# Optimization experiments

Hardware: AMD Instinct MI355X
Metric: run time of the kernel (lower is better)

Reference implementation:

```python
import jax, jax.numpy as jnp
import numpy as np

N_NODES = 2048
N_EDGES = 8192
EDGE_DIM = 10
EDGE_HIDDEN = 32
HID = 160


def nnconv(x, edge_index, edge_attr, w1, b1, w2, b2, root, bias):
    """PyG-style NNConv with aggr='mean'.
    x: [N, HID], edge_attr: [E, EDGE_DIM], edge_index: [2, E] (src, dst).
    Per-edge weight W_e = MLP(e) reshaped to [HID, HID]; message = x[src] @ W_e,
    mean-aggregated at dst, plus root transform and bias.
    """
    n = x.shape[0]
    h = jax.nn.relu(edge_attr @ w1 + b1)                     # [E, EDGE_HIDDEN]
    W = (h @ w2 + b2).reshape(-1, HID, HID)                  # [E, HID, HID]
    src, dst = edge_index[0], edge_index[1]
    msg = jnp.einsum('ei,eio->eo', x[src], W)                # [E, HID]
    summed = jax.ops.segment_sum(msg, dst, num_segments=n)   # [N, HID]
    cnt = jax.ops.segment_sum(jnp.ones((msg.shape[0],), x.dtype), dst,
                              num_segments=n)
    aggr = summed / jnp.maximum(cnt, 1.0)[:, None]           # mean; 0 for isolated
    return aggr + x @ root + bias


def setup_inputs() -> dict:
    key = jax.random.key(0)
    ks = jax.random.split(key, 16)
    s = 1.0 / np.sqrt(HID)
    se = 1.0 / np.sqrt(EDGE_DIM)
    sh = 1.0 / np.sqrt(EDGE_HIDDEN)
    inp = {
        'x': jax.random.normal(ks[0], (N_NODES, HID), jnp.float32),
        'edge_attr': jax.random.uniform(ks[1], (N_EDGES, EDGE_DIM), jnp.float32),
        # conv1 (subgraph_conv1) params
        'w1_a': jax.random.normal(ks[2], (EDGE_DIM, EDGE_HIDDEN), jnp.float32) * se,
        'b1_a': jnp.zeros((EDGE_HIDDEN,), jnp.float32),
        'w2_a': jax.random.normal(ks[3], (EDGE_HIDDEN, HID * HID), jnp.float32) * sh,
        'b2_a': jnp.zeros((HID * HID,), jnp.float32),
        'root_a': jax.random.normal(ks[4], (HID, HID), jnp.float32) * s,
        'bias_a': jnp.zeros((HID,), jnp.float32),
        # conv2 (subgraph_conv2, applied twice) params
        'w1_b': jax.random.normal(ks[5], (EDGE_DIM, EDGE_HIDDEN), jnp.float32) * se,
        'b1_b': jnp.zeros((EDGE_HIDDEN,), jnp.float32),
        'w2_b': jax.random.normal(ks[6], (EDGE_HIDDEN, HID * HID), jnp.float32) * sh,
        'b2_b': jnp.zeros((HID * HID,), jnp.float32),
        'root_b': jax.random.normal(ks[7], (HID, HID), jnp.float32) * s,
        'bias_b': jnp.zeros((HID,), jnp.float32),
        'edge_index': jax.random.randint(ks[8], (2, N_EDGES), 0, N_NODES, jnp.int64),
    }
    return inp


def reference(x, edge_attr, w1_a, b1_a, w2_a, b2_a, root_a, bias_a,
              w1_b, b1_b, w2_b, b2_b, root_b, bias_b, edge_index):
    # subgraph_conv1 -> ReLU -> subgraph_conv2 -> ReLU -> subgraph_conv2
    h = jax.nn.relu(nnconv(x, edge_index, edge_attr,
                           w1_a, b1_a, w2_a, b2_a, root_a, bias_a))
    h = jax.nn.relu(nnconv(h, edge_index, edge_attr,
                           w1_b, b1_b, w2_b, b2_b, root_b, bias_b))
    h = nnconv(h, edge_index, edge_attr,
               w1_b, b1_b, w2_b, b2_b, root_b, bias_b)
    return h
```

## Files before the change

### kernel.cpp

```cpp
#include <hip/hip_runtime.h>

#define NN 2048
#define NE 8192
#define ED 10
#define EH 32
#define HID 160
#define KT 5440
#define KS 10
#define KSTEPS 17

typedef __attribute__((ext_vector_type(8))) short short8;
typedef __attribute__((ext_vector_type(4))) float f32x4;
typedef unsigned int u32;

__device__ __forceinline__ ushort f2bf(float v) {
    u32 u = __float_as_uint(v);
    u += 0x7FFF + ((u >> 16) & 1);
    return (ushort)(u >> 16);
}
__device__ __forceinline__ float bf2f(ushort u) {
    return __uint_as_float(((u32)u) << 16);
}
__device__ __forceinline__ void gl2lds16(const ushort* g, ushort* l) {
    __builtin_amdgcn_global_load_lds(
        (const __attribute__((address_space(1))) u32*)g,
        (__attribute__((address_space(3))) u32*)l, 16, 0, 0);
}

__global__ __launch_bounds__(256) void k_prep(
        const float* __restrict__ x, ushort* __restrict__ xb,
        const float* __restrict__ ea,
        const float* __restrict__ w1a, const float* __restrict__ b1a,
        const float* __restrict__ w1b, const float* __restrict__ b1b,
        float* __restrict__ ha, float* __restrict__ hb,
        const float* __restrict__ w2a, const float* __restrict__ b2a,
        const float* __restrict__ roota,
        const float* __restrict__ w2b, const float* __restrict__ b2b,
        const float* __restrict__ rootb,
        ushort* __restrict__ WcA, ushort* __restrict__ WcB,
        const int* __restrict__ ei, int* __restrict__ doff,
        int* __restrict__ degg, float* __restrict__ dinv,
        int* __restrict__ delist) {
    __shared__ __align__(16) char smem[21760];
    int b = blockIdx.x, t = threadIdx.x;

    if (b < 512) {
        int set = b >> 8, rel = b & 255;
        const float* w1 = set ? w1b : w1a;
        const float* b1 = set ? b1b : b1a;
        float* h = set ? hb : ha;
        int idx = rel * 1024 + t * 4;
        int e = idx >> 5, j0 = idx & 31;
        float o4[4];
#pragma unroll
        for (int u = 0; u < 4; ++u) {
            float acc = b1[j0 + u];
#pragma unroll
            for (int i = 0; i < ED; ++i) acc += ea[e * ED + i] * w1[i * EH + j0 + u];
            o4[u] = fmaxf(acc, 0.f);
        }
        *(float4*)&h[idx] = *(const float4*)o4;
        return;
    }
    if (b < 672) {
        int rel = b - 512;
        int set = rel / 80, i0 = (rel % 80) * 2;
        u32 (*tile)[34] = (u32(*)[34])smem;
        const float* w2 = set ? w2b : w2a;
        const float* b2 = set ? b2b : b2a;
        const float* root = set ? rootb : roota;
        ushort* W = set ? WcB : WcA;
        if (t < HID) {
#pragma unroll
            for (int di = 0; di < 2; ++di) {
                int i = i0 + di;
#pragma unroll
                for (int p = 0; p < 16; ++p) {
                    float v0 = w2[(size_t)(2 * p) * 25600 + i * HID + t];
                    float v1 = w2[(size_t)(2 * p + 1) * 25600 + i * HID + t];
                    tile[t][di * 17 + p] = ((u32)f2bf(v1) << 16) | f2bf(v0);
                }
                tile[t][di * 17 + 16] = ((u32)f2bf(root[i * HID + t]) << 16) |
                                        f2bf(b2[i * HID + t]);
            }
        }
        __syncthreads();
        u32* dst = (u32*)W;
        for (int w = t; w < 5440; w += 256) {
            int o = w / 34, j = w - o * 34;
            dst[(size_t)o * 2720 + i0 * 17 + j] = tile[o][j];
        }
        return;
    }
    if (b < 992) {
        int idx = (b - 672) * 1024 + t * 4;
        float4 xv = *(const float4*)&x[idx];
        ushort o4[4] = {f2bf(xv.x), f2bf(xv.y), f2bf(xv.z), f2bf(xv.w)};
        *(u32*)&xb[idx] = *(const u32*)&o4[0];
        *(u32*)&xb[idx + 2] = *(const u32*)&o4[2];
        return;
    }
    int* deg = (int*)smem;
    int* cur = deg + NN;
    int* part = cur + NN;
    for (int i = t; i < NN; i += 256) deg[i] = 0;
    __syncthreads();
    for (int e = t; e < NE; e += 256) atomicAdd(&deg[ei[NE + e]], 1);
    __syncthreads();
    int loc[8], s = 0;
#pragma unroll
    for (int i = 0; i < 8; ++i) { loc[i] = s; s += deg[t * 8 + i]; }
    part[t] = s;
    __syncthreads();
    int tot = s;
    for (int st = 1; st < 256; st <<= 1) {
        int v = (t >= st) ? part[t - st] : 0;
        __syncthreads();
        part[t] += v;
        __syncthreads();
    }
    int base = part[t] - tot;
#pragma unroll
    for (int i = 0; i < 8; ++i) {
        int d = t * 8 + i;
        doff[d] = base + loc[i];
        cur[d] = base + loc[i];
        degg[d] = deg[d];
        dinv[d] = 1.0f / fmaxf((float)deg[d], 1.0f);
    }
    __syncthreads();
    for (int e = t; e < NE; e += 256) {
        int d = ei[NE + e];
        int p = atomicAdd(&cur[d], 1);
        delist[p] = e;
    }
}

__global__ __launch_bounds__(160) void k_scatter(
        const ushort* __restrict__ xb, const float* __restrict__ h,
        const int* __restrict__ ei, const int* __restrict__ doff,
        const int* __restrict__ degg, const float* __restrict__ dinv,
        const int* __restrict__ delist, ushort* __restrict__ T) {
    __shared__ float hbuf[32 * EH];
    __shared__ int ebuf[32], sbuf[32];
    __shared__ u32 rowbuf[KT / 2];
    int d = blockIdx.x, t = threadIdx.x;
    int o0 = doff[d], dg = degg[d];
    float acc[33];
#pragma unroll
    for (int q = 0; q < 33; ++q) acc[q] = 0.f;
    for (int c0 = 0; c0 < dg; c0 += 32) {
        int nc = min(32, dg - c0);
        __syncthreads();
        if (t < nc) {
            int e = delist[o0 + c0 + t];
            ebuf[t] = e;
            sbuf[t] = ei[e];
        }
        __syncthreads();
        for (int i = t; i < nc * EH; i += 160)
            hbuf[i] = h[(size_t)ebuf[i >> 5] * EH + (i & 31)];
        __syncthreads();
        for (int j = 0; j < nc; ++j) {
            float xs = bf2f(xb[(size_t)sbuf[j] * HID + t]);
            const float* hj = &hbuf[j * EH];
#pragma unroll
            for (int q = 0; q < 32; ++q) acc[q] += hj[q] * xs;
            acc[32] += xs;
        }
    }
    float di = dinv[d];
#pragma unroll
    for (int p = 0; p < 16; ++p)
        rowbuf[t * 17 + p] = ((u32)f2bf(acc[2 * p + 1] * di) << 16) |
                             f2bf(acc[2 * p] * di);
    rowbuf[t * 17 + 16] = ((u32)xb[(size_t)d * HID + t] << 16) | f2bf(acc[32] * di);
    __syncthreads();
    u32* Trow = (u32*)(T + (size_t)d * KT);
    for (int w = t; w < KT / 2; w += 160) Trow[w] = rowbuf[w];
}

__global__ __launch_bounds__(256) void k_out(const ushort* __restrict__ A,
                                             const ushort* __restrict__ B,
                                             float* __restrict__ Cp) {
    __shared__ ushort sA[2][128 * 32], sB[2][160 * 32];
    int tid = threadIdx.x;
    int bm = blockIdx.x * 128, ks = blockIdx.y;
    int k0base = ks * (KT / KS);
    int wid = tid >> 6, lane = tid & 63;
    int wm = (wid >> 1) * 64, wn = (wid & 1) * 80;
    int lr = lane & 15, lk = lane >> 4;
    f32x4 acc[4][5];
#pragma unroll
    for (int i = 0; i < 4; ++i)
#pragma unroll
        for (int j = 0; j < 5; ++j) acc[i][j] = (f32x4){0.f, 0.f, 0.f, 0.f};

    auto stage = [&](int buf, int c) {
        int k0 = k0base + c * 32;
#pragma unroll
        for (int i = 0; i < 2; ++i) {
            int s = tid + i * 256;
            int r = s >> 2, go = (s & 3) * 8;
            gl2lds16(&A[(size_t)(bm + r) * KT + k0 + go], &sA[buf][s * 8]);
        }
#pragma unroll
        for (int i = 0; i < 2; ++i) {
            int s = tid + i * 256;
            int r = s >> 2, go = (s & 3) * 8;
            gl2lds16(&B[(size_t)r * KT + k0 + go], &sB[buf][s * 8]);
        }
        if (tid < 128) {
            int s = tid + 512;
            int r = s >> 2, go = (s & 3) * 8;
            gl2lds16(&B[(size_t)r * KT + k0 + go], &sB[buf][s * 8]);
        }
    };
    stage(0, 0);
    __syncthreads();
    for (int c = 0; c < KSTEPS; ++c) {
        int cur = c & 1;
        if (c + 1 < KSTEPS) stage(cur ^ 1, c + 1);
        short8 av[4], bv[5];
#pragma unroll
        for (int mt = 0; mt < 4; ++mt)
            av[mt] = *(const short8*)&sA[cur][(wm + mt * 16 + lr) * 32 + lk * 8];
#pragma unroll
        for (int nt = 0; nt < 5; ++nt)
            bv[nt] = *(const short8*)&sB[cur][(wn + nt * 16 + lr) * 32 + lk * 8];
#pragma unroll
        for (int mt = 0; mt < 4; ++mt)
#pragma unroll
            for (int nt = 0; nt < 5; ++nt)
                acc[mt][nt] = __builtin_amdgcn_mfma_f32_16x16x32_bf16(
                    av[mt], bv[nt], acc[mt][nt], 0, 0, 0);
        __syncthreads();
    }
    float* Cb = Cp + (size_t)ks * NN * HID;
#pragma unroll
    for (int mt = 0; mt < 4; ++mt)
#pragma unroll
        for (int nt = 0; nt < 5; ++nt) {
            int m0 = bm + wm + mt * 16 + lk * 4;
            int n = wn + nt * 16 + lr;
#pragma unroll
            for (int r = 0; r < 4; ++r)
                Cb[(size_t)(m0 + r) * HID + n] = acc[mt][nt][r];
        }
}

__global__ __launch_bounds__(160) void k_fin(const float* __restrict__ Cp,
        const float* __restrict__ bias, ushort* __restrict__ xn,
        float* __restrict__ out, int last) {
    int d = blockIdx.x, t = threadIdx.x;
    float s = bias[t];
#pragma unroll
    for (int p = 0; p < KS; ++p) s += Cp[(size_t)p * NN * HID + d * HID + t];
    if (last) out[d * HID + t] = s;
    else      xn[d * HID + t] = f2bf(fmaxf(s, 0.f));
}

extern "C" void kernel_launch(void* const* d_in, const int* in_sizes, int n_in,
                              void* d_out, int out_size, void* d_ws, size_t ws_size,
                              hipStream_t stream) {
    const float* x     = (const float*)d_in[0];
    const float* ea    = (const float*)d_in[1];
    const float* w1a   = (const float*)d_in[2];
    const float* b1a   = (const float*)d_in[3];
    const float* w2a   = (const float*)d_in[4];
    const float* b2a   = (const float*)d_in[5];
    const float* roota = (const float*)d_in[6];
    const float* biasa = (const float*)d_in[7];
    const float* w1b   = (const float*)d_in[8];
    const float* b1b   = (const float*)d_in[9];
    const float* w2b   = (const float*)d_in[10];
    const float* b2b   = (const float*)d_in[11];
    const float* rootb = (const float*)d_in[12];
    const float* biasb = (const float*)d_in[13];
    const int*   ei    = (const int*)d_in[14];
    float* out = (float*)d_out;

    char* p = (char*)d_ws;
    ushort* T   = (ushort*)p;  p += (size_t)NN * KT * 2;
    ushort* WcA = (ushort*)p;  p += (size_t)HID * KT * 2;
    ushort* WcB = (ushort*)p;  p += (size_t)HID * KT * 2;
    float* Cp   = (float*)p;   p += (size_t)KS * NN * HID * 4;
    float* h_a  = (float*)p;   p += (size_t)NE * EH * 4;
    float* h_b  = (float*)p;   p += (size_t)NE * EH * 4;
    ushort* xb0 = (ushort*)p;  p += (size_t)NN * HID * 2;
    ushort* xn  = (ushort*)p;  p += (size_t)NN * HID * 2;
    int* doff   = (int*)p;     p += NN * 4;
    int* degg   = (int*)p;     p += NN * 4;
    float* dinv = (float*)p;   p += NN * 4;
    int* delist = (int*)p;     p += NE * 4;

    k_prep<<<993, 256, 0, stream>>>(x, xb0, ea, w1a, b1a, w1b, b1b, h_a, h_b,
                                    w2a, b2a, roota, w2b, b2b, rootb, WcA, WcB,
                                    ei, doff, degg, dinv, delist);

    struct Layer { const ushort *xin, *wc; const float *h, *bias; int last; };
    Layer L[3] = {
        {xb0, WcA, h_a, biasa, 0},
        {xn,  WcB, h_b, biasb, 0},
        {xn,  WcB, h_b, biasb, 1},
    };
    for (int l = 0; l < 3; ++l) {
        k_scatter<<<NN, 160, 0, stream>>>(L[l].xin, L[l].h, ei, doff, degg,
                                          dinv, delist, T);
        k_out<<<dim3(NN / 128, KS), 256, 0, stream>>>(T, L[l].wc, Cp);
        k_fin<<<NN, 160, 0, stream>>>(Cp, L[l].bias, xn, out, L[l].last);
    }
}
```

Before: 201.1 us.

## Fuse scatter, GEMM and finalize into one per-layer kernel split by K-slices

Replaces the per-layer scatter + GEMM + finalize chain with a single kernel per layer. Each block handles 32 destination nodes and one 16-wide input-channel slice. It builds its slice of the aggregated A operand directly in LDS and runs the MFMA GEMM against the streamed weight slice, writing K-split partials. The next layer reconstructs its input by summing the previous partials plus bias and ReLU during the gather, which removes the large T intermediate and the bf16 x buffers. The cost is that the gather now reads ten fp32 partials per source element, and each block only does a 32-row GEMM that re-streams the weights.

```diff
diff --git a/kernel.cpp b/kernel.cpp
--- a/kernel.cpp
+++ b/kernel.cpp
@@ -7,7 +7,10 @@
 #define HID 160
 #define KT 5440
 #define KS 10
-#define KSTEPS 17
+#define KSL 544
+#define MT 32
+#define APAD 552
+#define NNH (NN * HID)
 
 typedef __attribute__((ext_vector_type(8))) short short8;
 typedef __attribute__((ext_vector_type(4))) float f32x4;
@@ -21,14 +24,26 @@
 __device__ __forceinline__ float bf2f(ushort u) {
     return __uint_as_float(((u32)u) << 16);
 }
+__device__ __forceinline__ u32 packbf(float lo, float hi) {
+    return ((u32)f2bf(hi) << 16) | f2bf(lo);
+}
 __device__ __forceinline__ void gl2lds16(const ushort* g, ushort* l) {
     __builtin_amdgcn_global_load_lds(
         (const __attribute__((address_space(1))) u32*)g,
         (__attribute__((address_space(3))) u32*)l, 16, 0, 0);
 }
 
+__device__ __forceinline__ float gatherx(const float* __restrict__ x0,
+                                         const float* __restrict__ cpin,
+                                         float biasv, int node, int i) {
+    if (x0) return x0[node * HID + i];
+    float s = biasv;
+#pragma unroll
+    for (int p = 0; p < KS; ++p) s += cpin[(size_t)p * NNH + node * HID + i];
+    return fmaxf(s, 0.f);
+}
+
 __global__ __launch_bounds__(256) void k_prep(
-        const float* __restrict__ x, ushort* __restrict__ xb,
         const float* __restrict__ ea,
         const float* __restrict__ w1a, const float* __restrict__ b1a,
         const float* __restrict__ w1b, const float* __restrict__ b1b,
@@ -78,10 +93,9 @@
                 for (int p = 0; p < 16; ++p) {
                     float v0 = w2[(size_t)(2 * p) * 25600 + i * HID + t];
                     float v1 = w2[(size_t)(2 * p + 1) * 25600 + i * HID + t];
-                    tile[t][di * 17 + p] = ((u32)f2bf(v1) << 16) | f2bf(v0);
+                    tile[t][di * 17 + p] = packbf(v0, v1);
                 }
-                tile[t][di * 17 + 16] = ((u32)f2bf(root[i * HID + t]) << 16) |
-                                        f2bf(b2[i * HID + t]);
+                tile[t][di * 17 + 16] = packbf(b2[i * HID + t], root[i * HID + t]);
             }
         }
         __syncthreads();
@@ -90,14 +104,6 @@
             int o = w / 34, j = w - o * 34;
             dst[(size_t)o * 2720 + i0 * 17 + j] = tile[o][j];
         }
-        return;
-    }
-    if (b < 992) {
-        int idx = (b - 672) * 1024 + t * 4;
-        float4 xv = *(const float4*)&x[idx];
-        ushort o4[4] = {f2bf(xv.x), f2bf(xv.y), f2bf(xv.z), f2bf(xv.w)};
-        *(u32*)&xb[idx] = *(const u32*)&o4[0];
-        *(u32*)&xb[idx + 2] = *(const u32*)&o4[2];
         return;
     }
     int* deg = (int*)smem;
@@ -136,128 +142,139 @@
     }
 }
 
-__global__ __launch_bounds__(160) void k_scatter(
-        const ushort* __restrict__ xb, const float* __restrict__ h,
+__global__ __launch_bounds__(256) void k_layer(
+        const float* __restrict__ x0,
+        const float* __restrict__ cpin,
+        const float* __restrict__ bprev,
+        const float* __restrict__ h, const ushort* __restrict__ wc,
         const int* __restrict__ ei, const int* __restrict__ doff,
         const int* __restrict__ degg, const float* __restrict__ dinv,
-        const int* __restrict__ delist, ushort* __restrict__ T) {
-    __shared__ float hbuf[32 * EH];
-    __shared__ int ebuf[32], sbuf[32];
-    __shared__ u32 rowbuf[KT / 2];
-    int d = blockIdx.x, t = threadIdx.x;
-    int o0 = doff[d], dg = degg[d];
-    float acc[33];
-#pragma unroll
-    for (int q = 0; q < 33; ++q) acc[q] = 0.f;
-    for (int c0 = 0; c0 < dg; c0 += 32) {
-        int nc = min(32, dg - c0);
+        const int* __restrict__ delist, float* __restrict__ cpout) {
+    __shared__ __align__(16) ushort sA[MT * APAD];
+    __shared__ __align__(16) ushort sB[2][160 * 32];
+    __shared__ float hbuf[128 * 33];
+    __shared__ int ebuf[128], sbuf[128];
+    int t = threadIdx.x;
+    int bm = blockIdx.x, ks = blockIdx.y;
+    int d0 = bm * MT, i0 = ks * 16;
+    int e0 = doff[d0];
+    int e1 = (d0 + MT < NN) ? doff[d0 + MT] : NE;
+
+    int il = t & 15, i = i0 + il;
+    int dA = d0 + (t >> 4), dB = dA + 16;
+    float biasv = x0 ? 0.f : bprev[i];
+    int aLo = doff[dA], aHi = aLo + degg[dA];
+    int bLo = doff[dB], bHi = bLo + degg[dB];
+    float accA[33], accB[33];
+#pragma unroll
+    for (int q = 0; q < 33; ++q) { accA[q] = 0.f; accB[q] = 0.f; }
+
+    for (int c0 = e0; c0 < e1; c0 += 128) {
+        int nc = min(128, e1 - c0);
         __syncthreads();
         if (t < nc) {
-            int e = delist[o0 + c0 + t];
+            int e = delist[c0 + t];
             ebuf[t] = e;
             sbuf[t] = ei[e];
         }
         __syncthreads();
-        for (int i = t; i < nc * EH; i += 160)
-            hbuf[i] = h[(size_t)ebuf[i >> 5] * EH + (i & 31)];
-        __syncthreads();
-        for (int j = 0; j < nc; ++j) {
-            float xs = bf2f(xb[(size_t)sbuf[j] * HID + t]);
-            const float* hj = &hbuf[j * EH];
-#pragma unroll
-            for (int q = 0; q < 32; ++q) acc[q] += hj[q] * xs;
-            acc[32] += xs;
-        }
-    }
-    float di = dinv[d];
-#pragma unroll
-    for (int p = 0; p < 16; ++p)
-        rowbuf[t * 17 + p] = ((u32)f2bf(acc[2 * p + 1] * di) << 16) |
-                             f2bf(acc[2 * p] * di);
-    rowbuf[t * 17 + 16] = ((u32)xb[(size_t)d * HID + t] << 16) | f2bf(acc[32] * di);
-    __syncthreads();
-    u32* Trow = (u32*)(T + (size_t)d * KT);
-    for (int w = t; w < KT / 2; w += 160) Trow[w] = rowbuf[w];
-}
-
-__global__ __launch_bounds__(256) void k_out(const ushort* __restrict__ A,
-                                             const ushort* __restrict__ B,
-                                             float* __restrict__ Cp) {
-    __shared__ ushort sA[2][128 * 32], sB[2][160 * 32];
-    int tid = threadIdx.x;
-    int bm = blockIdx.x * 128, ks = blockIdx.y;
-    int k0base = ks * (KT / KS);
-    int wid = tid >> 6, lane = tid & 63;
-    int wm = (wid >> 1) * 64, wn = (wid & 1) * 80;
-    int lr = lane & 15, lk = lane >> 4;
-    f32x4 acc[4][5];
-#pragma unroll
-    for (int i = 0; i < 4; ++i)
-#pragma unroll
-        for (int j = 0; j < 5; ++j) acc[i][j] = (f32x4){0.f, 0.f, 0.f, 0.f};
+        for (int idx = t; idx < nc * 32; idx += 256)
+            hbuf[(idx >> 5) * 33 + (idx & 31)] =
+                h[(size_t)ebuf[idx >> 5] * EH + (idx & 31)];
+        __syncthreads();
+        int jl = max(aLo, c0) - c0, jh = min(aHi, c0 + nc) - c0;
+        for (int j = jl; j < jh; ++j) {
+            float xs = gatherx(x0, cpin, biasv, sbuf[j], i);
+            const float* hj = &hbuf[j * 33];
+#pragma unroll
+            for (int q = 0; q < 32; ++q) accA[q] += hj[q] * xs;
+            accA[32] += xs;
+        }
+        jl = max(bLo, c0) - c0; jh = min(bHi, c0 + nc) - c0;
+        for (int j = jl; j < jh; ++j) {
+            float xs = gatherx(x0, cpin, biasv, sbuf[j], i);
+            const float* hj = &hbuf[j * 33];
+#pragma unroll
+            for (int q = 0; q < 32; ++q) accB[q] += hj[q] * xs;
+            accB[32] += xs;
+        }
+    }
+    float rootA = gatherx(x0, cpin, biasv, dA, i);
+    float rootB = gatherx(x0, cpin, biasv, dB, i);
 
     auto stage = [&](int buf, int c) {
-        int k0 = k0base + c * 32;
-#pragma unroll
-        for (int i = 0; i < 2; ++i) {
-            int s = tid + i * 256;
+        size_t k0 = (size_t)ks * KSL + c * 32;
+#pragma unroll
+        for (int q = 0; q < 2; ++q) {
+            int s = t + q * 256;
             int r = s >> 2, go = (s & 3) * 8;
-            gl2lds16(&A[(size_t)(bm + r) * KT + k0 + go], &sA[buf][s * 8]);
-        }
-#pragma unroll
-        for (int i = 0; i < 2; ++i) {
-            int s = tid + i * 256;
+            gl2lds16(&wc[(size_t)r * KT + k0 + go], &sB[buf][s * 8]);
+        }
+        if (t < 128) {
+            int s = t + 512;
             int r = s >> 2, go = (s & 3) * 8;
-            gl2lds16(&B[(size_t)r * KT + k0 + go], &sB[buf][s * 8]);
-        }
-        if (tid < 128) {
-            int s = tid + 512;
-            int r = s >> 2, go = (s & 3) * 8;
-            gl2lds16(&B[(size_t)r * KT + k0 + go], &sB[buf][s * 8]);
+            gl2lds16(&wc[(size_t)r * KT + k0 + go], &sB[buf][s * 8]);
         }
     };
     stage(0, 0);
-    __syncthreads();
-    for (int c = 0; c < KSTEPS; ++c) {
+
+    {
+        float diA = dinv[dA], diB = dinv[dB];
+        u32* pa = (u32*)&sA[(t >> 4) * APAD + il * 34];
+        u32* pb = (u32*)&sA[((t >> 4) + 16) * APAD + il * 34];
+#pragma unroll
+        for (int p = 0; p < 16; ++p) {
+            pa[p] = packbf(accA[2 * p] * diA, accA[2 * p + 1] * diA);
+            pb[p] = packbf(accB[2 * p] * diB, accB[2 * p + 1] * diB);
+        }
+        pa[16] = packbf(accA[32] * diA, rootA);
+        pb[16] = packbf(accB[32] * diB, rootB);
+    }
+    __syncthreads();
+
+    int wid = t >> 6, lane = t & 63;
+    int wm = (wid >> 1) * 16, wn = (wid & 1) * 80;
+    int lr = lane & 15, lk = lane >> 4;
+    f32x4 acc[5];
+#pragma unroll
+    for (int j = 0; j < 5; ++j) acc[j] = (f32x4){0.f, 0.f, 0.f, 0.f};
+
+    for (int c = 0; c < 17; ++c) {
         int cur = c & 1;
-        if (c + 1 < KSTEPS) stage(cur ^ 1, c + 1);
-        short8 av[4], bv[5];
-#pragma unroll
-        for (int mt = 0; mt < 4; ++mt)
-            av[mt] = *(const short8*)&sA[cur][(wm + mt * 16 + lr) * 32 + lk * 8];
+        if (c + 1 < 17) stage(cur ^ 1, c + 1);
+        short8 av = *(const short8*)&sA[(wm + lr) * APAD + c * 32 + lk * 8];
+        short8 bv[5];
 #pragma unroll
         for (int nt = 0; nt < 5; ++nt)
             bv[nt] = *(const short8*)&sB[cur][(wn + nt * 16 + lr) * 32 + lk * 8];
 #pragma unroll
-        for (int mt = 0; mt < 4; ++mt)
-#pragma unroll
-            for (int nt = 0; nt < 5; ++nt)
-                acc[mt][nt] = __builtin_amdgcn_mfma_f32_16x16x32_bf16(
-                    av[mt], bv[nt], acc[mt][nt], 0, 0, 0);
-        __syncthreads();
-    }
-    float* Cb = Cp + (size_t)ks * NN * HID;
-#pragma unroll
-    for (int mt = 0; mt < 4; ++mt)
-#pragma unroll
-        for (int nt = 0; nt < 5; ++nt) {
-            int m0 = bm + wm + mt * 16 + lk * 4;
-            int n = wn + nt * 16 + lr;
-#pragma unroll
-            for (int r = 0; r < 4; ++r)
-                Cb[(size_t)(m0 + r) * HID + n] = acc[mt][nt][r];
-        }
-}
-
-__global__ __launch_bounds__(160) void k_fin(const float* __restrict__ Cp,
-        const float* __restrict__ bias, ushort* __restrict__ xn,
-        float* __restrict__ out, int last) {
-    int d = blockIdx.x, t = threadIdx.x;
-    float s = bias[t];
-#pragma unroll
-    for (int p = 0; p < KS; ++p) s += Cp[(size_t)p * NN * HID + d * HID + t];
-    if (last) out[d * HID + t] = s;
-    else      xn[d * HID + t] = f2bf(fmaxf(s, 0.f));
+        for (int nt = 0; nt < 5; ++nt)
+            acc[nt] = __builtin_amdgcn_mfma_f32_16x16x32_bf16(av, bv[nt], acc[nt], 0, 0, 0);
+        __syncthreads();
+    }
+
+    float* Cb = cpout + (size_t)ks * NNH;
+#pragma unroll
+    for (int nt = 0; nt < 5; ++nt) {
+        int n = wn + nt * 16 + lr;
+        int m0 = d0 + wm + lk * 4;
+#pragma unroll
+        for (int r = 0; r < 4; ++r)
+            Cb[(size_t)(m0 + r) * HID + n] = acc[nt][r];
+    }
+}
+
+__global__ __launch_bounds__(256) void k_fin(const float* __restrict__ Cp,
+                                             const float* __restrict__ bias,
+                                             float* __restrict__ out) {
+    int base = (blockIdx.x * 256 + threadIdx.x) * 4;
+    float4 s = *(const float4*)&bias[base % HID];
+#pragma unroll
+    for (int p = 0; p < KS; ++p) {
+        float4 v = *(const float4*)&Cp[(size_t)p * NNH + base];
+        s.x += v.x; s.y += v.y; s.z += v.z; s.w += v.w;
+    }
+    *(float4*)&out[base] = s;
 }
 
 extern "C" void kernel_launch(void* const* d_in, const int* in_sizes, int n_in,
@@ -281,33 +298,27 @@
     float* out = (float*)d_out;
 
     char* p = (char*)d_ws;
-    ushort* T   = (ushort*)p;  p += (size_t)NN * KT * 2;
+    float* Cp0  = (float*)p;   p += (size_t)KS * NNH * 4;
+    float* Cp1  = (float*)p;   p += (size_t)KS * NNH * 4;
     ushort* WcA = (ushort*)p;  p += (size_t)HID * KT * 2;
     ushort* WcB = (ushort*)p;  p += (size_t)HID * KT * 2;
-    float* Cp   = (float*)p;   p += (size_t)KS * NN * HID * 4;
     float* h_a  = (float*)p;   p += (size_t)NE * EH * 4;
     float* h_b  = (float*)p;   p += (size_t)NE * EH * 4;
-    ushort* xb0 = (ushort*)p;  p += (size_t)NN * HID * 2;
-    ushort* xn  = (ushort*)p;  p += (size_t)NN * HID * 2;
     int* doff   = (int*)p;     p += NN * 4;
     int* degg   = (int*)p;     p += NN * 4;
     float* dinv = (float*)p;   p += NN * 4;
     int* delist = (int*)p;     p += NE * 4;
 
-    k_prep<<<993, 256, 0, stream>>>(x, xb0, ea, w1a, b1a, w1b, b1b, h_a, h_b,
+    k_prep<<<673, 256, 0, stream>>>(ea, w1a, b1a, w1b, b1b, h_a, h_b,
                                     w2a, b2a, roota, w2b, b2b, rootb, WcA, WcB,
                                     ei, doff, degg, dinv, delist);
 
-    struct Layer { const ushort *xin, *wc; const float *h, *bias; int last; };
-    Layer L[3] = {
-        {xb0, WcA, h_a, biasa, 0},
-        {xn,  WcB, h_b, biasb, 0},
-        {xn,  WcB, h_b, biasb, 1},
-    };
-    for (int l = 0; l < 3; ++l) {
-        k_scatter<<<NN, 160, 0, stream>>>(L[l].xin, L[l].h, ei, doff, degg,
-                                          dinv, delist, T);
-        k_out<<<dim3(NN / 128, KS), 256, 0, stream>>>(T, L[l].wc, Cp);
-        k_fin<<<NN, 160, 0, stream>>>(Cp, L[l].bias, xn, out, L[l].last);
-    }
-}
+    dim3 lg(NN / MT, KS);
+    k_layer<<<lg, 256, 0, stream>>>(x, nullptr, nullptr, h_a, WcA,
+                                    ei, doff, degg, dinv, delist, Cp0);
+    k_layer<<<lg, 256, 0, stream>>>(nullptr, Cp0, biasa, h_b, WcB,
+                                    ei, doff, degg, dinv, delist, Cp1);
+    k_layer<<<lg, 256, 0, stream>>>(nullptr, Cp1, biasb, h_b, WcB,
+                                    ei, doff, degg, dinv, delist, Cp0);
+    k_fin<<<NNH / 1024, 256, 0, stream>>>(Cp0, biasb, out);
+}
```

Result: slower. 264.7 us (+31.6%).
